# Performance work log

Measured on AMD Instinct MI355X. Metric: run time of the kernel, lower is better.

## Reference

```python
import jax, jax.numpy as jnp
import numpy as np

D_MODEL = 2048
NUM_HEADS = 16
D_K = D_MODEL // NUM_HEADS

def setup_inputs() -> dict:
    key = jax.random.key(0)
    ks = jax.random.split(key, 5)
    scale = 1.0 / np.sqrt(D_MODEL)
    x = jax.random.normal(ks[0], (4, 2048, D_MODEL), dtype=jnp.float32)
    wq = jax.random.normal(ks[1], (D_MODEL, D_MODEL), dtype=jnp.float32) * scale
    wk = jax.random.normal(ks[2], (D_MODEL, D_MODEL), dtype=jnp.float32) * scale
    wv = jax.random.normal(ks[3], (D_MODEL, D_MODEL), dtype=jnp.float32) * scale
    wo = jax.random.normal(ks[4], (D_MODEL, D_MODEL), dtype=jnp.float32) * scale
    return {"x": x, "wq": wq, "wk": wk, "wv": wv, "wo": wo}

def reference(x, wq, wk, wv, wo):
    # torch Linear (no bias): y = x @ W^T
    B, S, _ = x.shape
    def split_heads(t):
        return t.reshape(B, S, NUM_HEADS, D_K).transpose(0, 2, 1, 3)  # [B,H,S,Dk]
    Q = split_heads(jnp.einsum('bsd,ed->bse', x, wq))
    K = split_heads(jnp.einsum('bsd,ed->bse', x, wk))
    V = split_heads(jnp.einsum('bsd,ed->bse', x, wv))
    scores = jnp.einsum('bhqd,bhkd->bhqk', Q, K) / jnp.sqrt(jnp.float32(D_K))
    attn = jax.nn.softmax(scores, axis=-1)  # dropout=0 (eval semantics)
    out = jnp.einsum('bhqk,bhkd->bhqd', attn, V)
    out = out.transpose(0, 2, 1, 3).reshape(B, S, D_MODEL)
    return jnp.einsum('bsd,ed->bse', out, wo)
```

## Files before the change

kernel.cpp:

```cpp
#include <hip/hip_runtime.h>
#include <math.h>

#define DMODEL 2048
#define NHEADS 16
#define DK     128
#define BATCH  4
#define SEQ    2048
#define MROWS  (BATCH*SEQ)

typedef unsigned short u16;
typedef short s16x8 __attribute__((ext_vector_type(8)));
typedef u16   u16x4 __attribute__((ext_vector_type(4)));
typedef u16   u16x8 __attribute__((ext_vector_type(8)));
typedef float f32x4 __attribute__((ext_vector_type(4)));
typedef unsigned int u32x4 __attribute__((ext_vector_type(4)));

#define MFMA16(a, b, c) __builtin_amdgcn_mfma_f32_16x16x32_bf16((a), (b), (c), 0, 0, 0)

__device__ __forceinline__ u16 f2bf(float f) {
    unsigned u = __builtin_bit_cast(unsigned, f);
    unsigned r = (u + 0x7fffu + ((u >> 16) & 1u)) >> 16;
    return (u16)r;
}
__device__ __forceinline__ float bf2f(u16 h) {
    unsigned u = ((unsigned)h) << 16;
    return __builtin_bit_cast(float, u);
}

__device__ __forceinline__ void gld_lds16(const u16* g, u16* l) {
    __builtin_amdgcn_global_load_lds(
        (const __attribute__((address_space(1))) unsigned int*)g,
        (__attribute__((address_space(3))) unsigned int*)l,
        16, 0, 0);
}

__global__ __launch_bounds__(256)
void split_bf16_kernel(const float* __restrict__ src,
                       u16* __restrict__ hi, u16* __restrict__ lo, int n8) {
    const int stride = gridDim.x * blockDim.x;
    for (int i = blockIdx.x * blockDim.x + threadIdx.x; i < n8; i += stride) {
        const float4 f0 = ((const float4*)src)[2 * i];
        const float4 f1 = ((const float4*)src)[2 * i + 1];
        const float f[8] = {f0.x, f0.y, f0.z, f0.w, f1.x, f1.y, f1.z, f1.w};
        u16x8 h8, l8;
#pragma unroll
        for (int j = 0; j < 8; ++j) {
            const u16 hb = f2bf(f[j]);
            h8[j] = hb;
            l8[j] = f2bf(f[j] - bf2f(hb));
        }
        ((u16x8*)hi)[i] = h8;
        ((u16x8*)lo)[i] = l8;
    }
}

__device__ __forceinline__ void gemm128_split_core(
        const u16* __restrict__ Ahg, const u16* __restrict__ Alg,
        const u16* __restrict__ Bhg, const u16* __restrict__ Blg,
        const int bm, const int bn, f32x4 (&acc)[4][4]) {
    __shared__ __align__(16) u16 Ah[128 * 32];
    __shared__ __align__(16) u16 Al[128 * 32];
    __shared__ __align__(16) u16 Bh[128 * 32];
    __shared__ __align__(16) u16 Bl[128 * 32];

    const int t    = threadIdx.x;
    const int lane = t & 63;
    const int wave = t >> 6;

    const int srow = t >> 2;
    const int skof = (t & 3) * 8;
    const size_t ga0 = (size_t)(bm + srow) * DMODEL + skof;
    const size_t ga1 = (size_t)(bm + srow + 64) * DMODEL + skof;
    const size_t gb0 = (size_t)(bn + srow) * DMODEL + skof;
    const size_t gb1 = (size_t)(bn + srow + 64) * DMODEL + skof;
    const int l0 = srow * 32 + skof;
    const int l1 = l0 + 64 * 32;

    const int lm = lane & 15;
    const int lg = lane >> 4;
    const int wr = (wave >> 1) * 64;
    const int wc = (wave & 1) * 64;
    const int aoff = (wr + lm) * 32 + lg * 8;
    const int boff = (wc + lm) * 32 + lg * 8;

    for (int kt = 0; kt < DMODEL; kt += 32) {
        __syncthreads();
        gld_lds16(Ahg + ga0 + kt, &Ah[l0]);
        gld_lds16(Ahg + ga1 + kt, &Ah[l1]);
        gld_lds16(Alg + ga0 + kt, &Al[l0]);
        gld_lds16(Alg + ga1 + kt, &Al[l1]);
        gld_lds16(Bhg + gb0 + kt, &Bh[l0]);
        gld_lds16(Bhg + gb1 + kt, &Bh[l1]);
        gld_lds16(Blg + gb0 + kt, &Bl[l0]);
        gld_lds16(Blg + gb1 + kt, &Bl[l1]);
        __syncthreads();

        s16x8 af[4], alf[4];
#pragma unroll
        for (int i = 0; i < 4; ++i) {
            af[i]  = *(const s16x8*)&Ah[aoff + i * 16 * 32];
            alf[i] = *(const s16x8*)&Al[aoff + i * 16 * 32];
        }
#pragma unroll
        for (int j = 0; j < 4; ++j) {
            const s16x8 bf  = *(const s16x8*)&Bh[boff + j * 16 * 32];
            const s16x8 blf = *(const s16x8*)&Bl[boff + j * 16 * 32];
#pragma unroll
            for (int i = 0; i < 4; ++i) {
                acc[i][j] = MFMA16(af[i],  bf,  acc[i][j]);
                acc[i][j] = MFMA16(alf[i], bf,  acc[i][j]);
                acc[i][j] = MFMA16(af[i],  blf, acc[i][j]);
            }
        }
    }
}

__global__ __launch_bounds__(256)
void qkv_proj_mfma(const u16* __restrict__ Xhi, const u16* __restrict__ Xlo,
                   const u16* __restrict__ Wh,  const u16* __restrict__ Wl,
                   u16* __restrict__ Qhi, u16* __restrict__ Qlo,
                   u16* __restrict__ Khi, u16* __restrict__ Klo,
                   u16* __restrict__ Vt) {
    const int g  = blockIdx.x >> 4;
    const int nb = blockIdx.x & 15;
    const int bm = blockIdx.y * 128;
    const size_t WE = (size_t)DMODEL * DMODEL;

    f32x4 acc[4][4] = {};
    gemm128_split_core(Xhi, Xlo, Wh + g * WE, Wl + g * WE, bm, nb * 128, acc);

    const int lane = threadIdx.x & 63;
    const int wave = threadIdx.x >> 6;
    const int lm = lane & 15;
    const int lg = lane >> 4;
    const int wr = (wave >> 1) * 64;
    const int wc = (wave & 1) * 64;

    if (g < 2) {
        u16* hiP = (g == 0) ? Qhi : Khi;
        u16* loP = (g == 0) ? Qlo : Klo;
        const float sc = (g == 0) ? 0.08838834764831845f : 1.0f;
#pragma unroll
        for (int i = 0; i < 4; ++i) {
#pragma unroll
            for (int r = 0; r < 4; ++r) {
                const int s  = bm + wr + i * 16 + lg * 4 + r;
                const int bb = s >> 11;
                const size_t base =
                    ((size_t)(bb * NHEADS + nb) * SEQ + (s & 2047)) * DK + wc + lm;
#pragma unroll
                for (int j = 0; j < 4; ++j) {
                    const float y = acc[i][j][r] * sc;
                    const u16 hb = f2bf(y);
                    hiP[base + j * 16] = hb;
                    loP[base + j * 16] = f2bf(y - bf2f(hb));
                }
            }
        }
    } else {
#pragma unroll
        for (int i = 0; i < 4; ++i) {
            const int s0 = bm + wr + i * 16 + lg * 4;
            const int bb = s0 >> 11;
            const int ss = s0 & 2047;
            const size_t rowb = (size_t)(bb * NHEADS + nb) * DK;
#pragma unroll
            for (int j = 0; j < 4; ++j) {
                u16x4 v;
#pragma unroll
                for (int r = 0; r < 4; ++r) v[r] = f2bf(acc[i][j][r]);
                *(u16x4*)(Vt + (rowb + wc + j * 16 + lm) * SEQ + ss) = v;
            }
        }
    }
}

__global__ __launch_bounds__(256)
void out_proj_mfma(const u16* __restrict__ Ohi, const u16* __restrict__ Olo,
                   const u16* __restrict__ Woh, const u16* __restrict__ Wol,
                   float* __restrict__ out) {
    const int bn = blockIdx.x * 128;
    const int bm = blockIdx.y * 128;
    f32x4 acc[4][4] = {};
    gemm128_split_core(Ohi, Olo, Woh, Wol, bm, bn, acc);

    const int lane = threadIdx.x & 63;
    const int wave = threadIdx.x >> 6;
    const int lm = lane & 15;
    const int lg = lane >> 4;
    const int wr = (wave >> 1) * 64;
    const int wc = (wave & 1) * 64;
#pragma unroll
    for (int i = 0; i < 4; ++i) {
#pragma unroll
        for (int r = 0; r < 4; ++r) {
            const int row = bm + wr + i * 16 + lg * 4 + r;
            float* dst = out + (size_t)row * DMODEL + bn + wc + lm;
#pragma unroll
            for (int j = 0; j < 4; ++j) dst[j * 16] = acc[i][j][r];
        }
    }
}

__global__ __launch_bounds__(256)
void attn_kernel(const u16* __restrict__ Qhi, const u16* __restrict__ Qlo,
                 const u16* __restrict__ KhiG, const u16* __restrict__ KloG,
                 const u16* __restrict__ VtG,
                 u16* __restrict__ Ohi, u16* __restrict__ Olo) {
    __shared__ u16 Khs[32][136];
    __shared__ u16 Kls[32][136];
    __shared__ u16 Vs[128][40];
    __shared__ unsigned int Pb[64][36];

    const int bh = blockIdx.y;
    const int q0 = blockIdx.x * 64;
    const int t  = threadIdx.x;
    const int l  = t & 63;
    const int w  = t >> 6;
    const int lm = l & 15;
    const int lg = l >> 4;
    const int woff = w * 16;

    s16x8 qh[4], ql[4];
    {
        const size_t qrow = (size_t)bh * SEQ + q0 + woff + lm;
#pragma unroll
        for (int kb = 0; kb < 4; ++kb) {
            const size_t off = qrow * DK + kb * 32 + lg * 8;
            qh[kb] = *(const s16x8*)(Qhi + off);
            ql[kb] = *(const s16x8*)(Qlo + off);
        }
    }

    f32x4 o[8];
#pragma unroll
    for (int nt = 0; nt < 8; ++nt) o[nt] = (f32x4){0.f, 0.f, 0.f, 0.f};
    float m[4] = {-1e30f, -1e30f, -1e30f, -1e30f};
    float lsm[4] = {0.f, 0.f, 0.f, 0.f};

    const int skey = t >> 3;
    const int sdb  = (t & 7) * 16;
    const int vdim = t >> 1;
    const int vkb  = (t & 1) * 16;
    const u16* Kh_base = KhiG + ((size_t)bh * SEQ + skey) * DK + sdb;
    const u16* Kl_base = KloG + ((size_t)bh * SEQ + skey) * DK + sdb;
    const u16* Vt_base = VtG + ((size_t)bh * DK + vdim) * SEQ + vkb;

    for (int kt = 0; kt < SEQ; kt += 32) {
        __syncthreads();
        {
            const u16* kh = Kh_base + (size_t)kt * DK;
            const u16* klp = Kl_base + (size_t)kt * DK;
            u16x8 a0 = *(const u16x8*)kh;
            u16x8 a1 = *(const u16x8*)(kh + 8);
            u16x8 b0 = *(const u16x8*)klp;
            u16x8 b1 = *(const u16x8*)(klp + 8);
            *(u16x8*)&Khs[skey][sdb]     = a0;
            *(u16x8*)&Khs[skey][sdb + 8] = a1;
            *(u16x8*)&Kls[skey][sdb]     = b0;
            *(u16x8*)&Kls[skey][sdb + 8] = b1;
            const u16* vp = Vt_base + kt;
            u16x8 v0 = *(const u16x8*)vp;
            u16x8 v1 = *(const u16x8*)(vp + 8);
            *(u16x8*)&Vs[vdim][vkb]     = v0;
            *(u16x8*)&Vs[vdim][vkb + 8] = v1;
        }
        __syncthreads();

        f32x4 sacc[2];
#pragma unroll
        for (int nt = 0; nt < 2; ++nt) {
            f32x4 acc = (f32x4){0.f, 0.f, 0.f, 0.f};
#pragma unroll
            for (int kb = 0; kb < 4; ++kb) {
                const s16x8 bh_f = *(const s16x8*)&Khs[nt * 16 + lm][kb * 32 + lg * 8];
                const s16x8 bl_f = *(const s16x8*)&Kls[nt * 16 + lm][kb * 32 + lg * 8];
                acc = MFMA16(qh[kb], bh_f, acc);
                acc = MFMA16(ql[kb], bh_f, acc);
                acc = MFMA16(qh[kb], bl_f, acc);
            }
            sacc[nt] = acc;
        }

        float corr[4], p0[4], p1[4];
#pragma unroll
        for (int r = 0; r < 4; ++r) {
            float v = fmaxf(sacc[0][r], sacc[1][r]);
            v = fmaxf(v, __shfl_xor(v, 1));
            v = fmaxf(v, __shfl_xor(v, 2));
            v = fmaxf(v, __shfl_xor(v, 4));
            v = fmaxf(v, __shfl_xor(v, 8));
            const float mnew = fmaxf(m[r], v);
            corr[r] = __expf(m[r] - mnew);
            m[r] = mnew;
            p0[r] = __expf(sacc[0][r] - mnew);
            p1[r] = __expf(sacc[1][r] - mnew);
            float ls = p0[r] + p1[r];
            ls += __shfl_xor(ls, 1);
            ls += __shfl_xor(ls, 2);
            ls += __shfl_xor(ls, 4);
            ls += __shfl_xor(ls, 8);
            lsm[r] = lsm[r] * corr[r] + ls;
        }
#pragma unroll
        for (int nt = 0; nt < 8; ++nt) {
#pragma unroll
            for (int r = 0; r < 4; ++r) o[nt][r] *= corr[r];
        }

#pragma unroll
        for (int r = 0; r < 4; ++r) {
            const int row = woff + lg * 4 + r;
            const u16 h0 = f2bf(p0[r]);
            const u16 l0 = f2bf(p0[r] - bf2f(h0));
            Pb[row][lm] = (unsigned)h0 | ((unsigned)l0 << 16);
            const u16 h1 = f2bf(p1[r]);
            const u16 l1 = f2bf(p1[r] - bf2f(h1));
            Pb[row][16 + lm] = (unsigned)h1 | ((unsigned)l1 << 16);
        }

        const u32x4 r0 = *(const u32x4*)&Pb[woff + lm][lg * 8];
        const u32x4 r1 = *(const u32x4*)&Pb[woff + lm][lg * 8 + 4];
        u32x4 phw, plw;
        phw[0] = (r0[0] & 0xffffu) | (r0[1] << 16);
        phw[1] = (r0[2] & 0xffffu) | (r0[3] << 16);
        phw[2] = (r1[0] & 0xffffu) | (r1[1] << 16);
        phw[3] = (r1[2] & 0xffffu) | (r1[3] << 16);
        plw[0] = (r0[0] >> 16) | (r0[1] & 0xffff0000u);
        plw[1] = (r0[2] >> 16) | (r0[3] & 0xffff0000u);
        plw[2] = (r1[0] >> 16) | (r1[1] & 0xffff0000u);
        plw[3] = (r1[2] >> 16) | (r1[3] & 0xffff0000u);
        const s16x8 pHf = __builtin_bit_cast(s16x8, phw);
        const s16x8 pLf = __builtin_bit_cast(s16x8, plw);

#pragma unroll
        for (int nt = 0; nt < 8; ++nt) {
            const s16x8 vf = *(const s16x8*)&Vs[nt * 16 + lm][lg * 8];
            o[nt] = MFMA16(pHf, vf, o[nt]);
            o[nt] = MFMA16(pLf, vf, o[nt]);
        }
    }

    const int bb = bh >> 4;
    const int hh = bh & 15;
    float inv[4];
#pragma unroll
    for (int r = 0; r < 4; ++r) inv[r] = 1.f / lsm[r];
#pragma unroll
    for (int nt = 0; nt < 8; ++nt) {
#pragma unroll
        for (int r = 0; r < 4; ++r) {
            const int qrow = q0 + woff + lg * 4 + r;
            const size_t idx =
                ((size_t)bb * SEQ + qrow) * DMODEL + hh * DK + nt * 16 + lm;
            const float y = o[nt][r] * inv[r];
            const u16 hb = f2bf(y);
            Ohi[idx] = hb;
            Olo[idx] = f2bf(y - bf2f(hb));
        }
    }
}

extern "C" void kernel_launch(void* const* d_in, const int* in_sizes, int n_in,
                              void* d_out, int out_size, void* d_ws, size_t ws_size,
                              hipStream_t stream) {
    const float* x  = (const float*)d_in[0];
    const float* wq = (const float*)d_in[1];
    const float* wk = (const float*)d_in[2];
    const float* wv = (const float*)d_in[3];
    const float* wo = (const float*)d_in[4];

    const size_t NE = (size_t)MROWS * DMODEL;
    const size_t WE = (size_t)DMODEL * DMODEL;

    u16* Qhi = (u16*)d_ws;
    u16* Qlo = Qhi + NE;
    u16* Khi = Qhi + 2 * NE;
    u16* Klo = Qhi + 3 * NE;
    u16* Vt  = Qhi + 4 * NE;
    u16* Wqkvh = Qhi + 5 * NE;
    u16* Wqkvl = Wqkvh + 3 * WE;
    u16* Ohi = Qhi + 5 * NE;
    u16* Olo = Ohi + NE;
    u16* Woh = Qhi;
    u16* Wol = Woh + WE;
    u16* Xhi = (u16*)d_out;
    u16* Xlo = Xhi + NE;

    dim3 blk(256);
    split_bf16_kernel<<<dim3(1024), blk, 0, stream>>>(x, Xhi, Xlo, (int)(NE / 8));
    split_bf16_kernel<<<dim3(512), blk, 0, stream>>>(wq, Wqkvh, Wqkvl, (int)(WE / 8));
    split_bf16_kernel<<<dim3(512), blk, 0, stream>>>(wk, Wqkvh + WE, Wqkvl + WE, (int)(WE / 8));
    split_bf16_kernel<<<dim3(512), blk, 0, stream>>>(wv, Wqkvh + 2 * WE, Wqkvl + 2 * WE, (int)(WE / 8));

    qkv_proj_mfma<<<dim3(48, 64), blk, 0, stream>>>(Xhi, Xlo, Wqkvh, Wqkvl,
                                                    Qhi, Qlo, Khi, Klo, Vt);
    attn_kernel<<<dim3(SEQ / 64, BATCH * NHEADS), blk, 0, stream>>>(
        Qhi, Qlo, Khi, Klo, Vt, Ohi, Olo);

    split_bf16_kernel<<<dim3(512), blk, 0, stream>>>(wo, Woh, Wol, (int)(WE / 8));
    out_proj_mfma<<<dim3(16, 64), blk, 0, stream>>>(Ohi, Olo, Woh, Wol, (float*)d_out);
}
```

Before: 1.575 ms.

## Prefetch next K/V tile into registers, swizzle attention blocks, truncate bf16 splits

The attention loop now issues global loads for the next K/V tile into registers before the barrier and writes the previously loaded tile to LDS, overlapping global latency with compute. Block indices are remapped so blocks sharing a head spread across the grid order, and launch bounds request 4 blocks per SM. The hi/lo bf16 split switches from round-to-nearest to truncation, which saves integer ops while the lo term still carries the residual. The risks are extra register pressure from the prefetch buffers under the occupancy hint and slightly different rounding of the split.

```diff
diff --git a/kernel.cpp b/kernel.cpp
--- a/kernel.cpp
+++ b/kernel.cpp
@@ -21,6 +21,9 @@
     unsigned u = __builtin_bit_cast(unsigned, f);
     unsigned r = (u + 0x7fffu + ((u >> 16) & 1u)) >> 16;
     return (u16)r;
+}
+__device__ __forceinline__ u16 f2bf_t(float f) {
+    return (u16)(__builtin_bit_cast(unsigned, f) >> 16);
 }
 __device__ __forceinline__ float bf2f(u16 h) {
     unsigned u = ((unsigned)h) << 16;
@@ -45,9 +48,9 @@
         u16x8 h8, l8;
 #pragma unroll
         for (int j = 0; j < 8; ++j) {
-            const u16 hb = f2bf(f[j]);
+            const u16 hb = f2bf_t(f[j]);
             h8[j] = hb;
-            l8[j] = f2bf(f[j] - bf2f(hb));
+            l8[j] = f2bf_t(f[j] - bf2f(hb));
         }
         ((u16x8*)hi)[i] = h8;
         ((u16x8*)lo)[i] = l8;
@@ -151,9 +154,9 @@
 #pragma unroll
                 for (int j = 0; j < 4; ++j) {
                     const float y = acc[i][j][r] * sc;
-                    const u16 hb = f2bf(y);
+                    const u16 hb = f2bf_t(y);
                     hiP[base + j * 16] = hb;
-                    loP[base + j * 16] = f2bf(y - bf2f(hb));
+                    loP[base + j * 16] = f2bf_t(y - bf2f(hb));
                 }
             }
         }
@@ -202,7 +205,7 @@
     }
 }
 
-__global__ __launch_bounds__(256)
+__global__ __launch_bounds__(256, 4)
 void attn_kernel(const u16* __restrict__ Qhi, const u16* __restrict__ Qlo,
                  const u16* __restrict__ KhiG, const u16* __restrict__ KloG,
                  const u16* __restrict__ VtG,
@@ -212,8 +215,11 @@
     __shared__ u16 Vs[128][40];
     __shared__ unsigned int Pb[64][36];
 
-    const int bh = blockIdx.y;
-    const int q0 = blockIdx.x * 64;
+    const int idlin = blockIdx.y * gridDim.x + blockIdx.x;
+    const int swz   = (idlin & 7) * 256 + (idlin >> 3);
+    const int bh    = swz >> 5;
+    const int q0    = (swz & 31) * 64;
+
     const int t  = threadIdx.x;
     const int l  = t & 63;
     const int w  = t >> 6;
@@ -246,25 +252,32 @@
     const u16* Kl_base = KloG + ((size_t)bh * SEQ + skey) * DK + sdb;
     const u16* Vt_base = VtG + ((size_t)bh * DK + vdim) * SEQ + vkb;
 
+    u16x8 pk0 = *(const u16x8*)(Kh_base);
+    u16x8 pk1 = *(const u16x8*)(Kh_base + 8);
+    u16x8 pl0 = *(const u16x8*)(Kl_base);
+    u16x8 pl1 = *(const u16x8*)(Kl_base + 8);
+    u16x8 pv0 = *(const u16x8*)(Vt_base);
+    u16x8 pv1 = *(const u16x8*)(Vt_base + 8);
+
     for (int kt = 0; kt < SEQ; kt += 32) {
+        const int ktn = (kt + 32 < SEQ) ? kt + 32 : 0;
+        const u16* khn = Kh_base + (size_t)ktn * DK;
+        const u16* kln = Kl_base + (size_t)ktn * DK;
+        const u16* vpn = Vt_base + ktn;
+        const u16x8 nk0 = *(const u16x8*)khn;
+        const u16x8 nk1 = *(const u16x8*)(khn + 8);
+        const u16x8 nl0 = *(const u16x8*)kln;
+        const u16x8 nl1 = *(const u16x8*)(kln + 8);
+        const u16x8 nv0 = *(const u16x8*)vpn;
+        const u16x8 nv1 = *(const u16x8*)(vpn + 8);
+
         __syncthreads();
-        {
-            const u16* kh = Kh_base + (size_t)kt * DK;
-            const u16* klp = Kl_base + (size_t)kt * DK;
-            u16x8 a0 = *(const u16x8*)kh;
-            u16x8 a1 = *(const u16x8*)(kh + 8);
-            u16x8 b0 = *(const u16x8*)klp;
-            u16x8 b1 = *(const u16x8*)(klp + 8);
-            *(u16x8*)&Khs[skey][sdb]     = a0;
-            *(u16x8*)&Khs[skey][sdb + 8] = a1;
-            *(u16x8*)&Kls[skey][sdb]     = b0;
-            *(u16x8*)&Kls[skey][sdb + 8] = b1;
-            const u16* vp = Vt_base + kt;
-            u16x8 v0 = *(const u16x8*)vp;
-            u16x8 v1 = *(const u16x8*)(vp + 8);
-            *(u16x8*)&Vs[vdim][vkb]     = v0;
-            *(u16x8*)&Vs[vdim][vkb + 8] = v1;
-        }
+        *(u16x8*)&Khs[skey][sdb]     = pk0;
+        *(u16x8*)&Khs[skey][sdb + 8] = pk1;
+        *(u16x8*)&Kls[skey][sdb]     = pl0;
+        *(u16x8*)&Kls[skey][sdb + 8] = pl1;
+        *(u16x8*)&Vs[vdim][vkb]      = pv0;
+        *(u16x8*)&Vs[vdim][vkb + 8]  = pv1;
         __syncthreads();
 
         f32x4 sacc[2];
@@ -311,11 +324,11 @@
 #pragma unroll
         for (int r = 0; r < 4; ++r) {
             const int row = woff + lg * 4 + r;
-            const u16 h0 = f2bf(p0[r]);
-            const u16 l0 = f2bf(p0[r] - bf2f(h0));
+            const u16 h0 = f2bf_t(p0[r]);
+            const u16 l0 = f2bf_t(p0[r] - bf2f(h0));
             Pb[row][lm] = (unsigned)h0 | ((unsigned)l0 << 16);
-            const u16 h1 = f2bf(p1[r]);
-            const u16 l1 = f2bf(p1[r] - bf2f(h1));
+            const u16 h1 = f2bf_t(p1[r]);
+            const u16 l1 = f2bf_t(p1[r] - bf2f(h1));
             Pb[row][16 + lm] = (unsigned)h1 | ((unsigned)l1 << 16);
         }
 
@@ -339,6 +352,8 @@
             o[nt] = MFMA16(pHf, vf, o[nt]);
             o[nt] = MFMA16(pLf, vf, o[nt]);
         }
+
+        pk0 = nk0; pk1 = nk1; pl0 = nl0; pl1 = nl1; pv0 = nv0; pv1 = nv1;
     }
 
     const int bb = bh >> 4;
@@ -354,9 +369,9 @@
             const size_t idx =
                 ((size_t)bb * SEQ + qrow) * DMODEL + hh * DK + nt * 16 + lm;
             const float y = o[nt][r] * inv[r];
-            const u16 hb = f2bf(y);
+            const u16 hb = f2bf_t(y);
             Ohi[idx] = hb;
-            Olo[idx] = f2bf(y - bf2f(hb));
+            Olo[idx] = f2bf_t(y - bf2f(hb));
         }
     }
 }
```

Measured after the change: 1.558 ms. Within noise of the previous version (-1.1%).
